# Kernel tuning notes

Measured on AMD Instinct MI355X. Metric: run time of the kernel, lower is better.

## Reference

```python
import jax, jax.numpy as jnp
import numpy as np

D = 1024
DFF = 4096
B, S = 4, 2048
EPS = 1e-6
SLOPE = 0.01  # torch LeakyReLU default


def setup_inputs() -> dict:
    key = jax.random.key(0)
    ks = jax.random.split(key, 16)
    sd = 1.0 / np.sqrt(D)
    sf = 1.0 / np.sqrt(DFF)
    return {
        "X": jax.random.normal(ks[0], (B, S, D), dtype=jnp.float32),
        "intensity": jax.random.uniform(ks[1], (B, S, S), dtype=jnp.float32),
        "Wq": jax.random.uniform(ks[2], (D, D), jnp.float32, -sd, sd),
        "bq": jax.random.uniform(ks[3], (D,), jnp.float32, -sd, sd),
        "Wk": jax.random.uniform(ks[4], (D, D), jnp.float32, -sd, sd),
        "bk": jax.random.uniform(ks[5], (D,), jnp.float32, -sd, sd),
        "Wv": jax.random.uniform(ks[6], (D, D), jnp.float32, -sd, sd),
        "bv": jax.random.uniform(ks[7], (D,), jnp.float32, -sd, sd),
        "Wo": jax.random.uniform(ks[8], (D, D), jnp.float32, -sd, sd),
        "bo": jax.random.uniform(ks[9], (D,), jnp.float32, -sd, sd),
        "W1": jax.random.uniform(ks[10], (D, DFF), jnp.float32, -sd, sd),
        "b1": jax.random.uniform(ks[11], (DFF,), jnp.float32, -sd, sd),
        "W2": jax.random.uniform(ks[12], (DFF, D), jnp.float32, -sf, sf),
        "b2": jax.random.uniform(ks[13], (D,), jnp.float32, -sf, sf),
        "g1": jnp.ones((D,), jnp.float32),
        "be1": jnp.zeros((D,), jnp.float32),
        "g2": jnp.ones((D,), jnp.float32),
        "be2": jnp.zeros((D,), jnp.float32),
    }


def _layernorm(x, g, b):
    mu = jnp.mean(x, axis=-1, keepdims=True)
    var = jnp.mean(jnp.square(x - mu), axis=-1, keepdims=True)
    return (x - mu) * jax.lax.rsqrt(var + EPS) * g + b


def reference(X, intensity, Wq, bq, Wk, bk, Wv, bv, Wo, bo, W1, b1, W2, b2, g1, be1, g2, be2):
    d_k = X.shape[-1]
    q = X @ Wq + bq
    k = X @ Wk + bk
    v = X @ Wv + bv
    # scores: [B,S,S]; scale applied to k^T as in source
    scores = jnp.einsum('bid,bjd->bij', q, k) / jnp.sqrt(jnp.float32(d_k))
    attn = jax.nn.softmax(scores, axis=-1) + intensity  # post-softmax bias add
    out = jnp.einsum('bij,bjd->bid', attn, v) @ Wo + bo
    h = _layernorm(out + X, g1, be1)
    ffn = jax.nn.leaky_relu(h @ W1 + b1, negative_slope=SLOPE) @ W2 + b2
    return _layernorm(ffn + h, g2, be2)
```

## Files before the change

### kernel.cpp

```cpp
#include <hip/hip_runtime.h>

#define B_   4
#define S_   2048
#define D_   1024
#define DFF_ 4096

typedef __attribute__((ext_vector_type(8))) short short8;
typedef __attribute__((ext_vector_type(4))) float floatx4;

__device__ __forceinline__ unsigned short f2b(float f) {
    unsigned int u = __float_as_uint(f);
    unsigned int r = (u + 0x7fffu + ((u >> 16) & 1u)) >> 16;
    return (unsigned short)r;
}
__device__ __forceinline__ float b2f(unsigned short u) {
    return __uint_as_float((unsigned int)u << 16);
}

__device__ __forceinline__ void swizzle_xy(int gx, int gy, int& bx, int& by) {
    if ((gy & 7) == 0) {
        const int linear = by * gx + bx;
        const int xcd = linear & 7;
        const int slot = linear >> 3;
        const int r = slot / gx;
        by = xcd * (gy >> 3) + r;
        bx = slot - r * gx;
    }
}

__device__ __forceinline__ void gemm_core256(
    const unsigned short* __restrict__ A,
    const unsigned short* __restrict__ Bt,
    int ldA, int ldB, int K, int m0, int n0,
    unsigned short* As, unsigned short* Bs,
    floatx4 acc[4][4])
{
    const int tid  = threadIdx.x;
    const int lane = tid & 63;
    const int wave = tid >> 6;

    const int ra = tid >> 3;
    const int pg = tid & 7;
    const int cg = (pg ^ (ra & 7)) * 8;
    const unsigned short* gA = A  + (long long)(m0 + ra) * ldA + cg;
    const unsigned short* gB = Bt + (long long)(n0 + ra) * ldB + cg;
    const long long pA = 64LL * ldA;
    const long long pB = 64LL * ldB;

    unsigned short* dA = As + wave * 512;
    unsigned short* dB = Bs + wave * 512;

    const int wr = (wave >> 1) * 64;
    const int wc = (wave & 1) * 64;
    const int fr = lane & 15;
    const int q  = lane >> 4;

    int aoff[2][4], boff[2][4];
#pragma unroll
    for (int h = 0; h < 2; h++)
#pragma unroll
        for (int i = 0; i < 4; i++) {
            const int rA = wr + i * 16 + fr;
            const int rB = wc + i * 16 + fr;
            const int g  = h * 4 + q;
            aoff[h][i] = rA * 64 + ((g ^ (rA & 7)) * 8);
            boff[h][i] = rB * 64 + ((g ^ (rB & 7)) * 8);
        }

    for (int k0 = 0; k0 < K; k0 += 64) {
        __syncthreads();
#pragma unroll
        for (int p = 0; p < 4; p++)
            __builtin_amdgcn_global_load_lds(
                (const __attribute__((address_space(1))) void*)(gA + k0 + p * pA),
                (__attribute__((address_space(3))) void*)(dA + p * 4096), 16, 0, 0);
#pragma unroll
        for (int p = 0; p < 2; p++)
            __builtin_amdgcn_global_load_lds(
                (const __attribute__((address_space(1))) void*)(gB + k0 + p * pB),
                (__attribute__((address_space(3))) void*)(dB + p * 4096), 16, 0, 0);
        __syncthreads();

#pragma unroll
        for (int h = 0; h < 2; h++) {
            short8 af[4], bfr[4];
#pragma unroll
            for (int mi = 0; mi < 4; mi++) af[mi] = *(const short8*)&As[aoff[h][mi]];
#pragma unroll
            for (int ni = 0; ni < 4; ni++) bfr[ni] = *(const short8*)&Bs[boff[h][ni]];
#pragma unroll
            for (int mi = 0; mi < 4; mi++)
#pragma unroll
                for (int ni = 0; ni < 4; ni++)
                    acc[mi][ni] = __builtin_amdgcn_mfma_f32_16x16x32_bf16(
                        af[mi], bfr[ni], acc[mi][ni], 0, 0, 0);
        }
    }
}

__global__ __launch_bounds__(256) void cast_bf16_kernel(
    const float4* __restrict__ src, ushort4* __restrict__ dst, int n4)
{
    int i = blockIdx.x * 256 + threadIdx.x;
    if (i < n4) {
        float4 f = src[i];
        ushort4 u;
        u.x = f2b(f.x); u.y = f2b(f.y); u.z = f2b(f.z); u.w = f2b(f.w);
        dst[i] = u;
    }
}

__global__ __launch_bounds__(256) void transpose_cast_kernel(
    const float* __restrict__ W, unsigned short* __restrict__ Wt, int K, int N)
{
    __shared__ float tile[32][33];
    const int tx = threadIdx.x;
    const int ty = threadIdx.y;
    const int bx = blockIdx.x * 32;
    const int by = blockIdx.y * 32;
#pragma unroll
    for (int j = 0; j < 32; j += 8)
        tile[ty + j][tx] = W[(long long)(by + ty + j) * N + bx + tx];
    __syncthreads();
#pragma unroll
    for (int j = 0; j < 32; j += 8)
        Wt[(long long)(bx + ty + j) * K + by + tx] = f2b(tile[tx][ty + j]);
}

__global__ __launch_bounds__(256) void vtrans_kernel(
    const unsigned short* __restrict__ Vb, unsigned short* __restrict__ Vt)
{
    __shared__ unsigned short tile[64][68];
    const int b  = blockIdx.z;
    const int s0 = blockIdx.y * 64;
    const int d0 = blockIdx.x * 64;
    const int tx = threadIdx.x & 15;
    const int ty = threadIdx.x >> 4;

    const unsigned short* src = Vb + ((long long)b * S_ + s0) * D_ + d0;
#pragma unroll
    for (int j = 0; j < 4; j++) {
        const int s = j * 16 + ty;
        ushort4 v = *(const ushort4*)(src + (long long)s * D_ + tx * 4);
        tile[tx * 4 + 0][s] = v.x;
        tile[tx * 4 + 1][s] = v.y;
        tile[tx * 4 + 2][s] = v.z;
        tile[tx * 4 + 3][s] = v.w;
    }
    __syncthreads();
    unsigned short* dst = Vt + ((long long)b * D_ + d0) * S_ + s0;
#pragma unroll
    for (int j = 0; j < 4; j++) {
        const int d = j * 16 + ty;
        ushort4 v;
        v.x = tile[d][tx * 4 + 0];
        v.y = tile[d][tx * 4 + 1];
        v.z = tile[d][tx * 4 + 2];
        v.w = tile[d][tx * 4 + 3];
        *(ushort4*)(dst + (long long)d * S_ + tx * 4) = v;
    }
}

template <int OUT_BF16, int ACT_LEAKY, int HAS_BIAS>
__global__ __launch_bounds__(512, 4) void gemm_bt(
    const unsigned short* __restrict__ A,
    const unsigned short* __restrict__ Bt,
    void* __restrict__ Cptr,
    const float* __restrict__ bias,
    int M, int N, int K, float scale,
    long long sA, long long sB, long long sC)
{
    __shared__ unsigned short As[256 * 64];
    __shared__ unsigned short Bs[128 * 64];

    const int lane = threadIdx.x & 63;
    const int wave = threadIdx.x >> 6;
    const int z    = blockIdx.z;

    int bx = blockIdx.x, by = blockIdx.y;
    swizzle_xy(gridDim.x, gridDim.y, bx, by);
    const int m0 = by * 256;
    const int n0 = bx * 128;

    floatx4 acc[4][4];
#pragma unroll
    for (int i = 0; i < 4; i++)
#pragma unroll
        for (int j = 0; j < 4; j++) acc[i][j] = floatx4{0.f, 0.f, 0.f, 0.f};

    gemm_core256(A + (long long)z * sA, Bt + (long long)z * sB,
                 K, K, K, m0, n0, As, Bs, acc);

    const int wr = (wave >> 1) * 64;
    const int wc = (wave & 1) * 64;
    const int cr = (lane >> 4) * 4;
    const int cc = lane & 15;
    float* Cf = (float*)Cptr;
    unsigned short* Cb = (unsigned short*)Cptr;

#pragma unroll
    for (int mi = 0; mi < 4; mi++) {
#pragma unroll
        for (int ni = 0; ni < 4; ni++) {
            const int col = n0 + wc + ni * 16 + cc;
            const float bv = HAS_BIAS ? bias[col] : 0.0f;
#pragma unroll
            for (int r = 0; r < 4; r++) {
                const int row = m0 + wr + mi * 16 + cr + r;
                float v = acc[mi][ni][r] * scale + bv;
                if (ACT_LEAKY) v = (v > 0.0f) ? v : 0.01f * v;
                const long long idx = (long long)z * sC + (long long)row * N + col;
                if (OUT_BF16) Cb[idx] = f2b(v); else Cf[idx] = v;
            }
        }
    }
}

template <int NK>
__global__ __launch_bounds__(512, 4) void gemm_bt_sk(
    const unsigned short* __restrict__ A,
    const unsigned short* __restrict__ Bt,
    unsigned short* __restrict__ P,
    int M, int N, int Kslice, int ldA, int ldB,
    long long sA, long long sB)
{
    __shared__ unsigned short As[256 * 64];
    __shared__ unsigned short Bs[128 * 64];

    const int lane = threadIdx.x & 63;
    const int wave = threadIdx.x >> 6;
    const int z    = blockIdx.z;
    const int ks   = z % NK;
    const int b    = z / NK;
    const int nb   = gridDim.z / NK;

    int bx = blockIdx.x, by = blockIdx.y;
    swizzle_xy(gridDim.x, gridDim.y, bx, by);
    const int m0 = by * 256;
    const int n0 = bx * 128;

    floatx4 acc[4][4];
#pragma unroll
    for (int i = 0; i < 4; i++)
#pragma unroll
        for (int j = 0; j < 4; j++) acc[i][j] = floatx4{0.f, 0.f, 0.f, 0.f};

    gemm_core256(A + (long long)b * sA + (long long)ks * Kslice,
                 Bt + (long long)b * sB + (long long)ks * Kslice,
                 ldA, ldB, Kslice, m0, n0, As, Bs, acc);

    const long long pbase = ((long long)ks * nb + b) * (long long)M * N;

    const int wr = (wave >> 1) * 64;
    const int wc = (wave & 1) * 64;
    const int cr = (lane >> 4) * 4;
    const int cc = lane & 15;

#pragma unroll
    for (int mi = 0; mi < 4; mi++) {
#pragma unroll
        for (int ni = 0; ni < 4; ni++) {
            const int col = n0 + wc + ni * 16 + cc;
#pragma unroll
            for (int r = 0; r < 4; r++) {
                const int row = m0 + wr + mi * 16 + cr + r;
                P[pbase + (long long)row * N + col] = f2b(acc[mi][ni][r]);
            }
        }
    }
}

__global__ __launch_bounds__(512, 4) void gemm_qkv(
    const unsigned short* __restrict__ A,
    const unsigned short* __restrict__ Bt,
    unsigned short* __restrict__ Qb,
    unsigned short* __restrict__ Kb,
    unsigned short* __restrict__ Vb,
    const float* __restrict__ bq,
    const float* __restrict__ bk,
    const float* __restrict__ bv)
{
    __shared__ unsigned short As[256 * 64];
    __shared__ unsigned short Bs[128 * 64];

    const int lane = threadIdx.x & 63;
    const int wave = threadIdx.x >> 6;

    int bx = blockIdx.x, by = blockIdx.y;
    swizzle_xy(gridDim.x, gridDim.y, bx, by);
    const int m0 = by * 256;
    const int n0 = bx * 128;

    floatx4 acc[4][4];
#pragma unroll
    for (int i = 0; i < 4; i++)
#pragma unroll
        for (int j = 0; j < 4; j++) acc[i][j] = floatx4{0.f, 0.f, 0.f, 0.f};

    gemm_core256(A, Bt, D_, D_, D_, m0, n0, As, Bs, acc);

    const int wr = (wave >> 1) * 64;
    const int wc = (wave & 1) * 64;
    const int cr = (lane >> 4) * 4;
    const int cc = lane & 15;

#pragma unroll
    for (int mi = 0; mi < 4; mi++) {
#pragma unroll
        for (int ni = 0; ni < 4; ni++) {
            const int col = n0 + wc + ni * 16 + cc;
            const int seg = col >> 10;
            const int c = col & 1023;
            const float* bp = (seg == 0) ? bq : ((seg == 1) ? bk : bv);
            unsigned short* dp = (seg == 0) ? Qb : ((seg == 1) ? Kb : Vb);
            const float bval = bp[c];
#pragma unroll
            for (int r = 0; r < 4; r++) {
                const int row = m0 + wr + mi * 16 + cr + r;
                dp[(long long)row * D_ + c] = f2b(acc[mi][ni][r] + bval);
            }
        }
    }
}

__global__ __launch_bounds__(256) void avred_kernel(
    const ushort4* __restrict__ p0, const ushort4* __restrict__ p1,
    ushort4* __restrict__ dst, int n4)
{
    int i = blockIdx.x * 256 + threadIdx.x;
    if (i < n4) {
        ushort4 a = p0[i], b = p1[i];
        ushort4 u;
        u.x = f2b(b2f(a.x) + b2f(b.x)); u.y = f2b(b2f(a.y) + b2f(b.y));
        u.z = f2b(b2f(a.z) + b2f(b.z)); u.w = f2b(b2f(a.w) + b2f(b.w));
        dst[i] = u;
    }
}

template <int HAS_OUTB>
__global__ __launch_bounds__(256) void ln_red_kernel(
    const unsigned short* __restrict__ p0, const unsigned short* __restrict__ p1,
    const float* __restrict__ resid, const float* __restrict__ bias,
    const float* __restrict__ g, const float* __restrict__ b,
    float* __restrict__ out_f, unsigned short* __restrict__ out_b)
{
    __shared__ float red[8];
    const long long row = blockIdx.x;
    const int tid = threadIdx.x;
    const ushort4 a0 = ((const ushort4*)(p0 + row * D_))[tid];
    const ushort4 a1 = ((const ushort4*)(p1 + row * D_))[tid];
    const float4 rv = ((const float4*)(resid + row * D_))[tid];
    const float4 bi = ((const float4*)bias)[tid];
    float v0 = b2f(a0.x) + b2f(a1.x) + bi.x + rv.x;
    float v1 = b2f(a0.y) + b2f(a1.y) + bi.y + rv.y;
    float v2 = b2f(a0.z) + b2f(a1.z) + bi.z + rv.z;
    float v3 = b2f(a0.w) + b2f(a1.w) + bi.w + rv.w;

    float s = v0 + v1 + v2 + v3;
#pragma unroll
    for (int o = 32; o > 0; o >>= 1) s += __shfl_xor(s, o);
    if ((tid & 63) == 0) red[tid >> 6] = s;
    __syncthreads();
    const float mean = (red[0] + red[1] + red[2] + red[3]) * (1.0f / D_);

    const float d0 = v0 - mean, d1 = v1 - mean, d2 = v2 - mean, d3 = v3 - mean;
    float q = d0 * d0 + d1 * d1 + d2 * d2 + d3 * d3;
#pragma unroll
    for (int o = 32; o > 0; o >>= 1) q += __shfl_xor(q, o);
    if ((tid & 63) == 0) red[4 + (tid >> 6)] = q;
    __syncthreads();
    const float var = (red[4] + red[5] + red[6] + red[7]) * (1.0f / D_);
    const float inv = rsqrtf(var + 1e-6f);

    const float4 gv = ((const float4*)g)[tid];
    const float4 bv = ((const float4*)b)[tid];
    const float o0 = d0 * inv * gv.x + bv.x;
    const float o1 = d1 * inv * gv.y + bv.y;
    const float o2 = d2 * inv * gv.z + bv.z;
    const float o3 = d3 * inv * gv.w + bv.w;

    ((float4*)(out_f + row * D_))[tid] = float4{o0, o1, o2, o3};
    if (HAS_OUTB) {
        ushort4 u; u.x = f2b(o0); u.y = f2b(o1); u.z = f2b(o2); u.w = f2b(o3);
        ((ushort4*)(out_b + row * D_))[tid] = u;
    }
}

__global__ __launch_bounds__(256) void softmax_bias_kernel(
    const unsigned short* __restrict__ scores, const float* __restrict__ intensity,
    unsigned short* __restrict__ attn)
{
    __shared__ float red[8];
    const long long row = blockIdx.x;
    const int tid = threadIdx.x;
    const ushort4* s4 = (const ushort4*)(scores + row * S_);
    const float4* i4 = (const float4*)(intensity + row * S_);
    ushort4* dst = (ushort4*)(attn + row * S_);

    float vv[8];
    {
        ushort4 a = s4[tid], b = s4[tid + 256];
        vv[0] = b2f(a.x); vv[1] = b2f(a.y); vv[2] = b2f(a.z); vv[3] = b2f(a.w);
        vv[4] = b2f(b.x); vv[5] = b2f(b.y); vv[6] = b2f(b.z); vv[7] = b2f(b.w);
    }

    float mx = vv[0];
#pragma unroll
    for (int i = 1; i < 8; i++) mx = fmaxf(mx, vv[i]);
#pragma unroll
    for (int o = 32; o > 0; o >>= 1) mx = fmaxf(mx, __shfl_xor(mx, o));
    if ((tid & 63) == 0) red[tid >> 6] = mx;
    __syncthreads();
    mx = fmaxf(fmaxf(red[0], red[1]), fmaxf(red[2], red[3]));

    float e[8];
    float sum = 0.f;
#pragma unroll
    for (int i = 0; i < 8; i++) { e[i] = __expf(vv[i] - mx); sum += e[i]; }
#pragma unroll
    for (int o = 32; o > 0; o >>= 1) sum += __shfl_xor(sum, o);
    if ((tid & 63) == 0) red[4 + (tid >> 6)] = sum;
    __syncthreads();
    sum = red[4] + red[5] + red[6] + red[7];
    const float rs = 1.0f / sum;

#pragma unroll
    for (int i = 0; i < 2; i++) {
        float4 iv = i4[tid + 256 * i];
        ushort4 o;
        o.x = f2b(e[4 * i + 0] * rs + iv.x);
        o.y = f2b(e[4 * i + 1] * rs + iv.y);
        o.z = f2b(e[4 * i + 2] * rs + iv.z);
        o.w = f2b(e[4 * i + 3] * rs + iv.w);
        dst[tid + 256 * i] = o;
    }
}

extern "C" void kernel_launch(void* const* d_in, const int* in_sizes, int n_in,
                              void* d_out, int out_size, void* d_ws, size_t ws_size,
                              hipStream_t stream)
{
    const float* X   = (const float*)d_in[0];
    const float* inten = (const float*)d_in[1];
    const float* Wq  = (const float*)d_in[2];
    const float* bq  = (const float*)d_in[3];
    const float* Wk  = (const float*)d_in[4];
    const float* bk  = (const float*)d_in[5];
    const float* Wv  = (const float*)d_in[6];
    const float* bv  = (const float*)d_in[7];
    const float* Wo  = (const float*)d_in[8];
    const float* bo  = (const float*)d_in[9];
    const float* W1  = (const float*)d_in[10];
    const float* b1  = (const float*)d_in[11];
    const float* W2  = (const float*)d_in[12];
    const float* b2  = (const float*)d_in[13];
    const float* g1  = (const float*)d_in[14];
    const float* be1 = (const float*)d_in[15];
    const float* g2  = (const float*)d_in[16];
    const float* be2 = (const float*)d_in[17];
    float* out = (float*)d_out;

    char* ws = (char*)d_ws;
    const size_t MB = 1ull << 20;
    unsigned short* Xb   = (unsigned short*)(ws + 0);
    unsigned short* Wqkv = (unsigned short*)(ws + 16 * MB);
    unsigned short* Wot  = (unsigned short*)(ws + 22 * MB);
    unsigned short* W1t  = (unsigned short*)(ws + 24 * MB);
    unsigned short* W2t  = (unsigned short*)(ws + 32 * MB);
    unsigned short* Qb   = (unsigned short*)(ws + 40 * MB);
    unsigned short* Kb   = (unsigned short*)(ws + 56 * MB);
    unsigned short* Vt   = (unsigned short*)(ws + 72 * MB);
    unsigned short* Sc   = (unsigned short*)(ws + 88 * MB);
    unsigned short* Vb   = (unsigned short*)(ws + 152 * MB);
    unsigned short* At   = (unsigned short*)(ws + 152 * MB);
    unsigned short* AVp  = (unsigned short*)(ws + 88 * MB);
    unsigned short* AVb  = (unsigned short*)(ws + 0);
    unsigned short* Op   = (unsigned short*)(ws + 152 * MB);
    float*          Hf   = (float*)(ws + 40 * MB);
    unsigned short* Hb   = (unsigned short*)(ws + 72 * MB);
    unsigned short* F1   = (unsigned short*)(ws + 88 * MB);
    unsigned short* Fp   = (unsigned short*)(ws + 152 * MB);

    const dim3 blk(256);
    const dim3 blk512(512);
    const dim3 tblk(32, 8);
    const long long MN_d = (long long)B_ * S_ * D_;

    cast_bf16_kernel<<<dim3(8192), blk, 0, stream>>>(
        (const float4*)X, (ushort4*)Xb, B_ * S_ * D_ / 4);
    transpose_cast_kernel<<<dim3(D_ / 32, D_ / 32), tblk, 0, stream>>>(
        Wq, Wqkv, D_, D_);
    transpose_cast_kernel<<<dim3(D_ / 32, D_ / 32), tblk, 0, stream>>>(
        Wk, Wqkv + 1024 * 1024, D_, D_);
    transpose_cast_kernel<<<dim3(D_ / 32, D_ / 32), tblk, 0, stream>>>(
        Wv, Wqkv + 2048 * 1024, D_, D_);
    transpose_cast_kernel<<<dim3(D_ / 32, D_ / 32), tblk, 0, stream>>>(Wo, Wot, D_, D_);
    transpose_cast_kernel<<<dim3(DFF_ / 32, D_ / 32), tblk, 0, stream>>>(W1, W1t, D_, DFF_);
    transpose_cast_kernel<<<dim3(D_ / 32, DFF_ / 32), tblk, 0, stream>>>(W2, W2t, DFF_, D_);

    gemm_qkv<<<dim3(24, 32), blk512, 0, stream>>>(Xb, Wqkv, Qb, Kb, Vb, bq, bk, bv);

    vtrans_kernel<<<dim3(D_ / 64, S_ / 64, B_), blk, 0, stream>>>(Vb, Vt);

    gemm_bt<1, 0, 0><<<dim3(16, 8, 4), blk512, 0, stream>>>(
        Qb, Kb, Sc, nullptr, S_, S_, D_, 0.03125f,
        (long long)S_ * D_, (long long)S_ * D_, (long long)S_ * S_);

    softmax_bias_kernel<<<dim3(B_ * S_), blk, 0, stream>>>(Sc, inten, At);

    gemm_bt_sk<2><<<dim3(8, 8, 8), blk512, 0, stream>>>(
        At, Vt, AVp, S_, D_, S_ / 2, S_, S_,
        (long long)S_ * S_, (long long)D_ * S_);
    avred_kernel<<<dim3(8192), blk, 0, stream>>>(
        (const ushort4*)AVp, (const ushort4*)(AVp + MN_d), (ushort4*)AVb,
        (int)(MN_d / 4));

    gemm_bt_sk<2><<<dim3(8, 32, 2), blk512, 0, stream>>>(
        AVb, Wot, Op, B_ * S_, D_, D_ / 2, D_, D_, 0, 0);

    ln_red_kernel<1><<<dim3(B_ * S_), blk, 0, stream>>>(
        Op, Op + MN_d, X, bo, g1, be1, Hf, Hb);

    gemm_bt<1, 1, 1><<<dim3(32, 32), blk512, 0, stream>>>(
        Hb, W1t, F1, b1, B_ * S_, DFF_, D_, 1.0f, 0, 0, 0);

    gemm_bt_sk<2><<<dim3(8, 32, 2), blk512, 0, stream>>>(
        F1, W2t, Fp, B_ * S_, D_, DFF_ / 2, DFF_, DFF_, 0, 0);

    ln_red_kernel<0><<<dim3(B_ * S_), blk, 0, stream>>>(
        Fp, Fp + MN_d, Hf, b2, g2, be2, out, nullptr);
}
```

Before: 560.1 us.

## Merge weight transposes into one launch and fold AV split-K reduction into Wo GEMM

The six weight transpose-cast launches become a single kernel that picks its matrix from the block index. The separate avred pass that summed the two AV split-K partials is removed. Instead the Wo GEMM runs over both partials, batched by pointer stride, and yields four partial outputs that the LayerNorm kernel now sums through a templated partial count. This drops launches and a full-size read-modify-write pass, but the Wo GEMM now does twice the work and the LN kernel reads twice as many partials.

Measured after the change: 563.7 us. Within noise of the previous version (+0.6%).

```diff
diff --git a/kernel.cpp b/kernel.cpp
--- a/kernel.cpp
+++ b/kernel.cpp
@@ -110,21 +110,46 @@
     }
 }
 
-__global__ __launch_bounds__(256) void transpose_cast_kernel(
-    const float* __restrict__ W, unsigned short* __restrict__ Wt, int K, int N)
+__device__ __forceinline__ void trans_tile(
+    const float* __restrict__ W, unsigned short* __restrict__ Wt,
+    int K, int N, int bx, int by, int tx, int ty)
 {
     __shared__ float tile[32][33];
-    const int tx = threadIdx.x;
-    const int ty = threadIdx.y;
-    const int bx = blockIdx.x * 32;
-    const int by = blockIdx.y * 32;
 #pragma unroll
     for (int j = 0; j < 32; j += 8)
-        tile[ty + j][tx] = W[(long long)(by + ty + j) * N + bx + tx];
+        tile[ty + j][tx] = W[(long long)(by * 32 + ty + j) * N + bx * 32 + tx];
     __syncthreads();
 #pragma unroll
     for (int j = 0; j < 32; j += 8)
-        Wt[(long long)(bx + ty + j) * K + by + tx] = f2b(tile[tx][ty + j]);
+        Wt[(long long)(bx * 32 + ty + j) * K + by * 32 + tx] = f2b(tile[tx][ty + j]);
+}
+
+__global__ __launch_bounds__(256) void transpose_all_kernel(
+    const float* __restrict__ Wq, const float* __restrict__ Wk,
+    const float* __restrict__ Wv, const float* __restrict__ Wo,
+    const float* __restrict__ W1, const float* __restrict__ W2,
+    unsigned short* __restrict__ Wqkv, unsigned short* __restrict__ Wot,
+    unsigned short* __restrict__ W1t, unsigned short* __restrict__ W2t)
+{
+    const int id = blockIdx.x;
+    const int tx = threadIdx.x & 31;
+    const int ty = threadIdx.x >> 5;
+    if (id < 4096) {
+        const int m = id >> 10;
+        const int t = id & 1023;
+        const int bx = t & 31, by = t >> 5;
+        const float* src = (m == 0) ? Wq : (m == 1) ? Wk : (m == 2) ? Wv : Wo;
+        unsigned short* dst = (m == 3) ? Wot : (Wqkv + (long long)m * 1024 * 1024);
+        trans_tile(src, dst, 1024, 1024, bx, by, tx, ty);
+    } else if (id < 8192) {
+        const int t = id - 4096;
+        const int bx = t & 127, by = t >> 7;
+        trans_tile(W1, W1t, 1024, 4096, bx, by, tx, ty);
+    } else {
+        const int t = id - 8192;
+        const int bx = t & 31, by = t >> 5;
+        trans_tile(W2, W2t, 4096, 1024, bx, by, tx, ty);
+    }
 }
 
 __global__ __launch_bounds__(256) void vtrans_kernel(
@@ -323,23 +348,9 @@
     }
 }
 
-__global__ __launch_bounds__(256) void avred_kernel(
-    const ushort4* __restrict__ p0, const ushort4* __restrict__ p1,
-    ushort4* __restrict__ dst, int n4)
-{
-    int i = blockIdx.x * 256 + threadIdx.x;
-    if (i < n4) {
-        ushort4 a = p0[i], b = p1[i];
-        ushort4 u;
-        u.x = f2b(b2f(a.x) + b2f(b.x)); u.y = f2b(b2f(a.y) + b2f(b.y));
-        u.z = f2b(b2f(a.z) + b2f(b.z)); u.w = f2b(b2f(a.w) + b2f(b.w));
-        dst[i] = u;
-    }
-}
-
-template <int HAS_OUTB>
+template <int NPART, int HAS_OUTB>
 __global__ __launch_bounds__(256) void ln_red_kernel(
-    const unsigned short* __restrict__ p0, const unsigned short* __restrict__ p1,
+    const unsigned short* __restrict__ p, long long pstride,
     const float* __restrict__ resid, const float* __restrict__ bias,
     const float* __restrict__ g, const float* __restrict__ b,
     float* __restrict__ out_f, unsigned short* __restrict__ out_b)
@@ -347,14 +358,14 @@
     __shared__ float red[8];
     const long long row = blockIdx.x;
     const int tid = threadIdx.x;
-    const ushort4 a0 = ((const ushort4*)(p0 + row * D_))[tid];
-    const ushort4 a1 = ((const ushort4*)(p1 + row * D_))[tid];
     const float4 rv = ((const float4*)(resid + row * D_))[tid];
     const float4 bi = ((const float4*)bias)[tid];
-    float v0 = b2f(a0.x) + b2f(a1.x) + bi.x + rv.x;
-    float v1 = b2f(a0.y) + b2f(a1.y) + bi.y + rv.y;
-    float v2 = b2f(a0.z) + b2f(a1.z) + bi.z + rv.z;
-    float v3 = b2f(a0.w) + b2f(a1.w) + bi.w + rv.w;
+    float v0 = bi.x + rv.x, v1 = bi.y + rv.y, v2 = bi.z + rv.z, v3 = bi.w + rv.w;
+#pragma unroll
+    for (int k = 0; k < NPART; k++) {
+        const ushort4 a = ((const ushort4*)(p + k * pstride + row * D_))[tid];
+        v0 += b2f(a.x); v1 += b2f(a.y); v2 += b2f(a.z); v3 += b2f(a.w);
+    }
 
     float s = v0 + v1 + v2 + v3;
 #pragma unroll
@@ -474,8 +485,7 @@
     unsigned short* Vb   = (unsigned short*)(ws + 152 * MB);
     unsigned short* At   = (unsigned short*)(ws + 152 * MB);
     unsigned short* AVp  = (unsigned short*)(ws + 88 * MB);
-    unsigned short* AVb  = (unsigned short*)(ws + 0);
-    unsigned short* Op   = (unsigned short*)(ws + 152 * MB);
+    unsigned short* Op   = (unsigned short*)(ws + 120 * MB);
     float*          Hf   = (float*)(ws + 40 * MB);
     unsigned short* Hb   = (unsigned short*)(ws + 72 * MB);
     unsigned short* F1   = (unsigned short*)(ws + 88 * MB);
@@ -483,20 +493,12 @@
 
     const dim3 blk(256);
     const dim3 blk512(512);
-    const dim3 tblk(32, 8);
     const long long MN_d = (long long)B_ * S_ * D_;
 
     cast_bf16_kernel<<<dim3(8192), blk, 0, stream>>>(
         (const float4*)X, (ushort4*)Xb, B_ * S_ * D_ / 4);
-    transpose_cast_kernel<<<dim3(D_ / 32, D_ / 32), tblk, 0, stream>>>(
-        Wq, Wqkv, D_, D_);
-    transpose_cast_kernel<<<dim3(D_ / 32, D_ / 32), tblk, 0, stream>>>(
-        Wk, Wqkv + 1024 * 1024, D_, D_);
-    transpose_cast_kernel<<<dim3(D_ / 32, D_ / 32), tblk, 0, stream>>>(
-        Wv, Wqkv + 2048 * 1024, D_, D_);
-    transpose_cast_kernel<<<dim3(D_ / 32, D_ / 32), tblk, 0, stream>>>(Wo, Wot, D_, D_);
-    transpose_cast_kernel<<<dim3(DFF_ / 32, D_ / 32), tblk, 0, stream>>>(W1, W1t, D_, DFF_);
-    transpose_cast_kernel<<<dim3(D_ / 32, DFF_ / 32), tblk, 0, stream>>>(W2, W2t, DFF_, D_);
+    transpose_all_kernel<<<dim3(12288), blk, 0, stream>>>(
+        Wq, Wk, Wv, Wo, W1, W2, Wqkv, Wot, W1t, W2t);
 
     gemm_qkv<<<dim3(24, 32), blk512, 0, stream>>>(Xb, Wqkv, Qb, Kb, Vb, bq, bk, bv);
 
@@ -511,15 +513,12 @@
     gemm_bt_sk<2><<<dim3(8, 8, 8), blk512, 0, stream>>>(
         At, Vt, AVp, S_, D_, S_ / 2, S_, S_,
         (long long)S_ * S_, (long long)D_ * S_);
-    avred_kernel<<<dim3(8192), blk, 0, stream>>>(
-        (const ushort4*)AVp, (const ushort4*)(AVp + MN_d), (ushort4*)AVb,
-        (int)(MN_d / 4));
-
-    gemm_bt_sk<2><<<dim3(8, 32, 2), blk512, 0, stream>>>(
-        AVb, Wot, Op, B_ * S_, D_, D_ / 2, D_, D_, 0, 0);
-
-    ln_red_kernel<1><<<dim3(B_ * S_), blk, 0, stream>>>(
-        Op, Op + MN_d, X, bo, g1, be1, Hf, Hb);
+
+    gemm_bt_sk<2><<<dim3(8, 32, 4), blk512, 0, stream>>>(
+        AVp, Wot, Op, B_ * S_, D_, D_ / 2, D_, D_, MN_d, 0);
+
+    ln_red_kernel<4, 1><<<dim3(B_ * S_), blk, 0, stream>>>(
+        Op, MN_d, X, bo, g1, be1, Hf, Hb);
 
     gemm_bt<1, 1, 1><<<dim3(32, 32), blk512, 0, stream>>>(
         Hb, W1t, F1, b1, B_ * S_, DFF_, D_, 1.0f, 0, 0, 0);
@@ -527,6 +526,6 @@
     gemm_bt_sk<2><<<dim3(8, 32, 2), blk512, 0, stream>>>(
         F1, W2t, Fp, B_ * S_, D_, DFF_ / 2, DFF_, DFF_, 0, 0);
 
-    ln_red_kernel<0><<<dim3(B_ * S_), blk, 0, stream>>>(
-        Fp, Fp + MN_d, Hf, b2, g2, be2, out, nullptr);
-}
+    ln_red_kernel<2, 0><<<dim3(B_ * S_), blk, 0, stream>>>(
+        Fp, MN_d, Hf, b2, g2, be2, out, nullptr);
+}
```
